# Optimization experiments

Measured on AMD Instinct MI355X. Metric: run time of the kernel, lower is better.

## Reference

```python
import jax, jax.numpy as jnp
import numpy as np

DEPTH, DIM, HEADS, MLP_HID, POS_DIM, PROJ_DIM, NCLS, INP = 5, 128, 8, 256, 128, 128, 1000, 35
EPS = 1e-5

def _ln(x, g, b):
    m = x.mean(-1, keepdims=True)
    v = ((x - m) ** 2).mean(-1, keepdims=True)
    return (x - m) / jnp.sqrt(v + EPS) * g + b

def _gelu(x):
    return jax.nn.gelu(x, approximate=False)  # torch nn.GELU default (erf)

def setup_inputs() -> dict:
    key = jax.random.key(0)
    ks = iter(jax.random.split(key, 80))
    nxt = lambda: next(ks)
    B, N = 8, 1024
    w = lambda *s: (jax.random.normal(nxt(), s, jnp.float32) / np.sqrt(s[-2]).astype(np.float32))
    z = lambda *s: jnp.zeros(s, jnp.float32)
    o = lambda *s: jnp.ones(s, jnp.float32)
    node_feat = jax.random.normal(nxt(), (B, N, 3), jnp.float32)
    a = (jax.random.uniform(nxt(), (B, N, N)) < 0.01).astype(jnp.float32)
    adj = jnp.maximum(a, a.transpose(0, 2, 1))  # symmetric 0/1 adjacency
    lapl = jax.random.normal(nxt(), (B, N, 32), jnp.float32) * 0.1
    d = dict(
        node_feat=node_feat, adj=adj, lapl=lapl,
        cls_token=jax.random.normal(nxt(), (1, 1, DIM), jnp.float32),
        pe_w1=w(INP, 2 * INP), pe_b1=z(2 * INP),
        pe_w2=w(2 * INP, 2 * INP), pe_b2=z(2 * INP),
        pe_w3=w(2 * INP, 2 * INP), pe_b3=z(2 * INP),
        pe_lng=o(2 * INP), pe_lnb=z(2 * INP),
        pe_w4=w(2 * INP, POS_DIM), pe_b4=z(POS_DIM),
        blk_ln1_g=o(DEPTH, DIM), blk_ln1_b=z(DEPTH, DIM),
        blk_qkv_w=w(DEPTH, DIM, 3 * HEADS * DIM),
        blk_proj_w=w(DEPTH, HEADS * DIM, DIM), blk_proj_b=z(DEPTH, DIM),
        blk_gamma_w=jax.random.uniform(nxt(), (DEPTH, DIM, 2), jnp.float32) * 0.01,
        blk_gamma_b=z(DEPTH, 2),
        blk_ln2_g=o(DEPTH, DIM), blk_ln2_b=z(DEPTH, DIM),
        blk_mlp_w1=w(DEPTH, DIM, MLP_HID), blk_mlp_b1=z(DEPTH, MLP_HID),
        blk_mlp_w2=w(DEPTH, MLP_HID, DIM), blk_mlp_b2=z(DEPTH, DIM),
        head_lng=o(DIM), head_lnb=z(DIM), head_w=w(DIM, DIM), head_b=z(DIM),
        proj_w1=w(DIM, PROJ_DIM), proj_b1=z(PROJ_DIM),
        proj_w2=w(PROJ_DIM, PROJ_DIM), proj_b2=z(PROJ_DIM),
        proj_w3=w(PROJ_DIM, PROJ_DIM), proj_b3=z(PROJ_DIM),
        proj_lng=o(PROJ_DIM), proj_lnb=z(PROJ_DIM),
        proj_w4=w(PROJ_DIM, NCLS), proj_b4=z(NCLS),
    )
    return d

def reference(node_feat, adj, lapl, cls_token, pe_w1, pe_b1, pe_w2, pe_b2, pe_w3, pe_b3,
              pe_lng, pe_lnb, pe_w4, pe_b4, blk_ln1_g, blk_ln1_b, blk_qkv_w, blk_proj_w,
              blk_proj_b, blk_gamma_w, blk_gamma_b, blk_ln2_g, blk_ln2_b, blk_mlp_w1,
              blk_mlp_b1, blk_mlp_w2, blk_mlp_b2, head_lng, head_lnb, head_w, head_b,
              proj_w1, proj_b1, proj_w2, proj_b2, proj_w3, proj_b3, proj_lng, proj_lnb,
              proj_w4, proj_b4):
    B, N, _ = node_feat.shape
    M = N + 1
    # positional-encoding MLP on concatenated [node_feat | lapl] (inp_dim = 35)
    x = jnp.concatenate([node_feat, lapl], axis=2)
    x = _gelu(x @ pe_w1 + pe_b1)
    x = _gelu(x @ pe_w2 + pe_b2)
    x = _gelu(x @ pe_w3 + pe_b3)
    x = _ln(x, pe_lng, pe_lnb) @ pe_w4 + pe_b4  # [B,N,DIM]
    x = jnp.concatenate([jnp.broadcast_to(cls_token, (B, 1, DIM)), x], axis=1)  # [B,M,DIM]
    # adjacency with cls row/col, adj_cls[:,0,0] = 1
    adj_cls = jnp.zeros((B, M, M), x.dtype).at[:, 0, 0].set(1.0).at[:, 1:, 1:].set(adj)
    scale = DIM ** (-0.5)
    for i in range(DEPTH):
        h = _ln(x, blk_ln1_g[i], blk_ln1_b[i])
        qkv = (h @ blk_qkv_w[i]).reshape(B, M, 3, HEADS, DIM).transpose(2, 0, 3, 1, 4)
        q, k, v = qkv[0], qkv[1], qkv[2]  # each [B,H,M,D]
        attn = jnp.einsum('bhnd,bhmd->bhnm', q, k) * scale
        gamma = jnp.exp(h @ blk_gamma_w[i] + blk_gamma_b[i])  # [B,M,2], use_exp=True
        attn = gamma[:, None, :, 0:1] * attn + gamma[:, None, :, 1:2] * adj_cls[:, None]
        attn = jax.nn.softmax(attn, axis=-1)
        o = jnp.einsum('bhnm,bhmd->bhnd', attn, v).transpose(0, 2, 1, 3).reshape(B, M, HEADS * DIM)
        x = o @ blk_proj_w[i] + blk_proj_b[i] + h  # residual from normed input (as in source)
        h2 = _ln(x, blk_ln2_g[i], blk_ln2_b[i])
        x = _gelu(h2 @ blk_mlp_w1[i] + blk_mlp_b1[i]) @ blk_mlp_w2[i] + blk_mlp_b2[i] + h2
    c = x[:, 0]
    c = _ln(c, head_lng, head_lnb) @ head_w + head_b  # mlp_head
    p = _gelu(c @ proj_w1 + proj_b1)
    p = _gelu(p @ proj_w2 + proj_b2)
    p = _gelu(p @ proj_w3 + proj_b3)
    p = _ln(p, proj_lng, proj_lnb) @ proj_w4 + proj_b4
    return (c, p)
```

## Files before the change

kernel.cpp:

```cpp
#include <hip/hip_runtime.h>
#include <hip/hip_bf16.h>
#include <math.h>

#define NB 8
#define NSEQ 1024
#define M_ 1025
#define ROWS (NB * M_)
#define DIMC 128
#define NHEADS 8
#define QKV3 3072
#define PEROWS (NB * NSEQ)
#define ACS 1088

typedef __attribute__((ext_vector_type(8))) short bf16x8;
typedef __attribute__((ext_vector_type(4))) float f32x4;

__device__ __forceinline__ float gelu_f(float x) {
  return 0.5f * x * (1.f + erff(x * 0.70710678118654752440f));
}

__device__ __forceinline__ unsigned short f2bf(float f) {
  __hip_bfloat16 h = __float2bfloat16(f);
  return *reinterpret_cast<unsigned short*>(&h);
}

__device__ __forceinline__ float bf2f(unsigned short u) {
  union { unsigned int i; float f; } c;
  c.i = ((unsigned int)u) << 16;
  return c.f;
}

template<int TR>
__global__ __launch_bounds__(256) void rowgemm_k(
    const float* __restrict__ in, const float* __restrict__ W,
    const float* __restrict__ bias, const float* __restrict__ res,
    float* __restrict__ out, int rows, int K, int Nout, int act, int remap)
{
  extern __shared__ float s_in[];
  const int tid = threadIdx.x;
  const int r0 = blockIdx.x * TR;
  const int tot = TR * K;
  for (int idx = tid; idx < tot; idx += blockDim.x) {
    int r = idx / K;
    int k = idx - r * K;
    int gr = r0 + r;
    s_in[idx] = (gr < rows) ? in[(size_t)gr * K + k] : 0.f;
  }
  __syncthreads();
  const int j = blockIdx.y * blockDim.x + tid;
  if (j >= Nout) return;
  float acc[TR];
  const float bv = bias ? bias[j] : 0.f;
#pragma unroll
  for (int r = 0; r < TR; ++r) acc[r] = bv;
  for (int k = 0; k < K; ++k) {
    const float w = W[(size_t)k * Nout + j];
#pragma unroll
    for (int r = 0; r < TR; ++r) acc[r] = fmaf(s_in[r * K + k], w, acc[r]);
  }
  for (int r = 0; r < TR; ++r) {
    const int gr = r0 + r;
    if (gr >= rows) break;
    float v = acc[r];
    if (act == 1) v = gelu_f(v);
    if (res) v += res[(size_t)gr * Nout + j];
    const size_t orow = remap ? (size_t)(gr + gr / 1024 + 1) : (size_t)gr;
    out[orow * (size_t)Nout + j] = v;
  }
}

template<int ACT, int OBF, int RES>
__global__ __launch_bounds__(256) void mgemm_k(
    const unsigned short* __restrict__ Xb, const unsigned short* __restrict__ Wt,
    const float* __restrict__ bias, const float* __restrict__ res,
    void* __restrict__ outp, int rows, int K, int N)
{
  __shared__ unsigned short sX[64][72];
  __shared__ unsigned short sW[64][72];
  const int tid = threadIdx.x;
  const int w = tid >> 6, lane = tid & 63;
  const int col = lane & 15, quad = lane >> 4;
  const int r0 = blockIdx.x * 64, n0 = blockIdx.y * 64;
  const int lr = tid >> 2, lc = tid & 3;
  const int xrow = min(r0 + lr, rows - 1);
  const unsigned short* xsrc = Xb + (size_t)xrow * K + lc * 8;
  const unsigned short* wsrc = Wt + (size_t)(n0 + lr) * K + lc * 8;

  f32x4 acc[4];
#pragma unroll
  for (int t = 0; t < 4; ++t) acc[t] = (f32x4){0.f, 0.f, 0.f, 0.f};

  for (int k0 = 0; k0 < K; k0 += 64) {
    __syncthreads();
    *(uint4*)&sX[lr][lc * 8]      = *(const uint4*)(xsrc + k0);
    *(uint4*)&sX[lr][lc * 8 + 32] = *(const uint4*)(xsrc + k0 + 32);
    *(uint4*)&sW[lr][lc * 8]      = *(const uint4*)(wsrc + k0);
    *(uint4*)&sW[lr][lc * 8 + 32] = *(const uint4*)(wsrc + k0 + 32);
    __syncthreads();
    const bf16x8 aX0 = *(const bf16x8*)&sX[w * 16 + col][quad * 8];
    const bf16x8 aX1 = *(const bf16x8*)&sX[w * 16 + col][32 + quad * 8];
#pragma unroll
    for (int t = 0; t < 4; ++t) {
      const bf16x8 bW0 = *(const bf16x8*)&sW[t * 16 + col][quad * 8];
      const bf16x8 bW1 = *(const bf16x8*)&sW[t * 16 + col][32 + quad * 8];
      acc[t] = __builtin_amdgcn_mfma_f32_16x16x32_bf16(aX0, bW0, acc[t], 0, 0, 0);
      acc[t] = __builtin_amdgcn_mfma_f32_16x16x32_bf16(aX1, bW1, acc[t], 0, 0, 0);
    }
  }
  const int gr_base = r0 + w * 16 + quad * 4;
#pragma unroll
  for (int t = 0; t < 4; ++t) {
    const int n = n0 + t * 16 + col;
    const float bv = bias ? bias[n] : 0.f;
#pragma unroll
    for (int r = 0; r < 4; ++r) {
      const int gr = gr_base + r;
      if (gr < rows) {
        float v = acc[t][r] + bv;
        if (ACT) v = gelu_f(v);
        if (RES) v += res[(size_t)gr * N + n];
        if (OBF) ((unsigned short*)outp)[(size_t)gr * N + n] = f2bf(v);
        else     ((float*)outp)[(size_t)gr * N + n] = v;
      }
    }
  }
}

__global__ __launch_bounds__(256) void ln_rows_k(
    const float* __restrict__ in, float* __restrict__ out,
    unsigned short* __restrict__ outb,
    const float* __restrict__ g, const float* __restrict__ b,
    const float* __restrict__ gw, const float* __restrict__ gb,
    float* __restrict__ gamout, int rows, int D)
{
  const int wv = (blockIdx.x * blockDim.x + threadIdx.x) >> 6;
  const int lane = threadIdx.x & 63;
  if (wv >= rows) return;
  const float* r = in + (size_t)wv * D;
  float s = 0.f;
  for (int d = lane; d < D; d += 64) s += r[d];
  for (int off = 32; off; off >>= 1) s += __shfl_down(s, off);
  const float mean = __shfl(s, 0) / (float)D;
  float v = 0.f;
  for (int d = lane; d < D; d += 64) { float t = r[d] - mean; v += t * t; }
  for (int off = 32; off; off >>= 1) v += __shfl_down(v, off);
  const float inv = rsqrtf(__shfl(v, 0) / (float)D + 1e-5f);
  float* orow = out + (size_t)wv * D;
  float a0 = 0.f, a1 = 0.f;
  for (int d = lane; d < D; d += 64) {
    const float o = (r[d] - mean) * inv * g[d] + b[d];
    orow[d] = o;
    if (outb) outb[(size_t)wv * D + d] = f2bf(o);
    if (gw) { a0 = fmaf(o, gw[2 * d], a0); a1 = fmaf(o, gw[2 * d + 1], a1); }
  }
  if (gw) {
    for (int off = 32; off; off >>= 1) { a0 += __shfl_down(a0, off); a1 += __shfl_down(a1, off); }
    if (lane == 0) {
      gamout[(size_t)wv * 2 + 0] = expf(a0 + gb[0]);
      gamout[(size_t)wv * 2 + 1] = expf(a1 + gb[1]);
    }
  }
}

__global__ void adjc_k(const float* __restrict__ adj, unsigned short* __restrict__ adjc)
{
  const int n = blockIdx.x;
  const int b = blockIdx.y;
  unsigned short* row = adjc + ((size_t)b * M_ + n) * ACS;
  const float* ar = (n >= 1) ? adj + ((size_t)b * NSEQ + (n - 1)) * NSEQ : nullptr;
  for (int m = threadIdx.x; m < ACS; m += 256) {
    float v = 0.f;
    if (n == 0) v = (m == 0) ? 1.f : 0.f;
    else if (m >= 1 && m <= NSEQ) v = ar[m - 1];
    row[m] = f2bf(v);
  }
}

__global__ void wtrans_k(const float* __restrict__ W, unsigned short* __restrict__ Wt,
                         int K, int N)
{
  __shared__ float t[32][33];
  const int k0 = blockIdx.x * 32, n0 = blockIdx.y * 32;
  const float* Wd = W + (size_t)blockIdx.z * K * N;
  unsigned short* Wtd = Wt + (size_t)blockIdx.z * K * N;
  for (int i = threadIdx.y; i < 32; i += 8)
    t[i][threadIdx.x] = Wd[(size_t)(k0 + i) * N + n0 + threadIdx.x];
  __syncthreads();
  for (int i = threadIdx.y; i < 32; i += 8)
    Wtd[(size_t)(n0 + i) * K + k0 + threadIdx.x] = f2bf(t[threadIdx.x][i]);
}

__global__ __launch_bounds__(256) void attn_mfma_k(
    const unsigned short* __restrict__ qkv, const float* __restrict__ gamma,
    const unsigned short* __restrict__ adjc, unsigned short* __restrict__ o)
{
  __shared__ unsigned short sK[64][136];
  __shared__ unsigned short sVt[128][72];
  __shared__ unsigned short sP[64][72];

  const int hh = blockIdx.x, qt = blockIdx.y, b = blockIdx.z;
  const int tid = threadIdx.x;
  const int w = tid >> 6;
  const int lane = tid & 63;
  const int col = lane & 15;
  const int quad = lane >> 4;
  const int n0 = qt * 64;
  const int qbase = n0 + w * 16;
  const float scale = 0.088388347648318447f;

  bf16x8 aQ[4];
  {
    const int qrow = min(qbase + col, 1024);
    const unsigned short* qp = qkv + ((size_t)(b * M_ + qrow)) * QKV3 + hh * DIMC + quad * 8;
#pragma unroll
    for (int c = 0; c < 4; ++c) aQ[c] = *(const bf16x8*)(qp + c * 32);
  }
  float g0[4], g1[4];
  const unsigned short* adjr[4];
#pragma unroll
  for (int r = 0; r < 4; ++r) {
    const int nc = min(qbase + quad * 4 + r, 1024);
    g0[r] = gamma[(size_t)(b * M_ + nc) * 2 + 0] * scale;
    g1[r] = gamma[(size_t)(b * M_ + nc) * 2 + 1];
    adjr[r] = adjc + ((size_t)b * M_ + nc) * ACS;
  }

  float l_i[4] = {0.f, 0.f, 0.f, 0.f};
  f32x4 Oacc[8];
#pragma unroll
  for (int t = 0; t < 8; ++t) Oacc[t] = (f32x4){0.f, 0.f, 0.f, 0.f};

  for (int kt = 0; kt < 17; ++kt) {
    const int m0 = kt * 64;
    __syncthreads();
#pragma unroll
    for (int l = 0; l < 4; ++l) {
      const int idx = l * 256 + tid;
      const int m = idx >> 4, c = idx & 15;
      const int gm = m0 + m;
      uint4 kv = make_uint4(0u, 0u, 0u, 0u), vv = make_uint4(0u, 0u, 0u, 0u);
      if (gm < M_) {
        const unsigned short* base = qkv + ((size_t)(b * M_ + gm)) * QKV3 + hh * DIMC + c * 8;
        kv = *(const uint4*)(base + 1024);
        vv = *(const uint4*)(base + 2048);
      }
      *(uint4*)&sK[m][c * 8] = kv;
      union { uint4 u; unsigned short s[8]; } vu; vu.u = vv;
      const int swcol = (((m >> 3) ^ (c & 7)) << 3) | (m & 7);
#pragma unroll
      for (int j = 0; j < 8; ++j) sVt[c * 8 + j][swcol] = vu.s[j];
    }
    __syncthreads();

    f32x4 Sacc[4];
#pragma unroll
    for (int t = 0; t < 4; ++t) Sacc[t] = (f32x4){0.f, 0.f, 0.f, 0.f};
#pragma unroll
    for (int t = 0; t < 4; ++t) {
#pragma unroll
      for (int c = 0; c < 4; ++c) {
        const bf16x8 bK = *(const bf16x8*)&sK[t * 16 + col][c * 32 + quad * 8];
        Sacc[t] = __builtin_amdgcn_mfma_f32_16x16x32_bf16(aQ[c], bK, Sacc[t], 0, 0, 0);
      }
    }

#pragma unroll
    for (int t = 0; t < 4; ++t) {
      const int m = m0 + t * 16 + col;
      const bool mv = (m < M_);
      const int chb = t * 2 + (col >> 3);
#pragma unroll
      for (int r = 0; r < 4; ++r) {
        const float av = bf2f(adjr[r][m]);
        const float s = fmaf(g0[r], Sacc[t][r], g1[r] * av);
        const float pv = mv ? __expf(s) : 0.f;
        l_i[r] += pv;
        const int ql = w * 16 + quad * 4 + r;
        sP[ql][((chb ^ (ql & 7)) * 8) + (col & 7)] = f2bf(pv);
      }
    }

#pragma unroll
    for (int ch = 0; ch < 2; ++ch) {
      const int r0a = w * 16 + col;
      const bf16x8 aP = *(const bf16x8*)&sP[r0a][(((ch * 4 + quad) ^ (col & 7)) * 8)];
#pragma unroll
      for (int t = 0; t < 8; ++t) {
        const int pc = (ch * 4 + quad) ^ ((t * 2 + (col >> 3)) & 7);
        const bf16x8 bV = *(const bf16x8*)&sVt[t * 16 + col][pc * 8];
        Oacc[t] = __builtin_amdgcn_mfma_f32_16x16x32_bf16(aP, bV, Oacc[t], 0, 0, 0);
      }
    }
  }

#pragma unroll
  for (int r = 0; r < 4; ++r) {
    float s = l_i[r];
    s += __shfl_xor(s, 1);
    s += __shfl_xor(s, 2);
    s += __shfl_xor(s, 4);
    s += __shfl_xor(s, 8);
    const int n = qbase + quad * 4 + r;
    if (n < M_) {
      const float invl = 1.f / s;
      unsigned short* orow = o + ((size_t)(b * M_ + n)) * (NHEADS * DIMC) + hh * DIMC + col;
#pragma unroll
      for (int t = 0; t < 8; ++t) orow[t * 16] = f2bf(Oacc[t][r] * invl);
    }
  }
}

__global__ void concat_pe_k(const float* __restrict__ nf, const float* __restrict__ lp,
                            float* __restrict__ x35, int rows)
{
  const int idx = blockIdx.x * blockDim.x + threadIdx.x;
  if (idx >= rows * 35) return;
  const int r = idx / 35, c = idx - r * 35;
  x35[idx] = (c < 3) ? nf[(size_t)r * 3 + c] : lp[(size_t)r * 32 + (c - 3)];
}

__global__ void fill_cls_k(const float* __restrict__ cls, float* __restrict__ x)
{
  x[(size_t)blockIdx.x * M_ * DIMC + threadIdx.x] = cls[threadIdx.x];
}

__global__ void extract_cls_k(const float* __restrict__ x, float* __restrict__ c0)
{
  c0[(size_t)blockIdx.x * DIMC + threadIdx.x] = x[(size_t)blockIdx.x * M_ * DIMC + threadIdx.x];
}

extern "C" void kernel_launch(void* const* d_in, const int* in_sizes, int n_in,
                              void* d_out, int out_size, void* d_ws, size_t ws_size,
                              hipStream_t stream)
{
  (void)in_sizes; (void)n_in; (void)out_size; (void)ws_size;
  const float* node_feat = (const float*)d_in[0];
  const float* adj       = (const float*)d_in[1];
  const float* lapl      = (const float*)d_in[2];
  const float* cls_token = (const float*)d_in[3];
  const float* pe_w1 = (const float*)d_in[4];
  const float* pe_b1 = (const float*)d_in[5];
  const float* pe_w2 = (const float*)d_in[6];
  const float* pe_b2 = (const float*)d_in[7];
  const float* pe_w3 = (const float*)d_in[8];
  const float* pe_b3 = (const float*)d_in[9];
  const float* pe_lng = (const float*)d_in[10];
  const float* pe_lnb = (const float*)d_in[11];
  const float* pe_w4 = (const float*)d_in[12];
  const float* pe_b4 = (const float*)d_in[13];
  const float* blk_ln1_g = (const float*)d_in[14];
  const float* blk_ln1_b = (const float*)d_in[15];
  const float* blk_qkv_w = (const float*)d_in[16];
  const float* blk_proj_w = (const float*)d_in[17];
  const float* blk_proj_b = (const float*)d_in[18];
  const float* blk_gamma_w = (const float*)d_in[19];
  const float* blk_gamma_b = (const float*)d_in[20];
  const float* blk_ln2_g = (const float*)d_in[21];
  const float* blk_ln2_b = (const float*)d_in[22];
  const float* blk_mlp_w1 = (const float*)d_in[23];
  const float* blk_mlp_b1 = (const float*)d_in[24];
  const float* blk_mlp_w2 = (const float*)d_in[25];
  const float* blk_mlp_b2 = (const float*)d_in[26];
  const float* head_lng = (const float*)d_in[27];
  const float* head_lnb = (const float*)d_in[28];
  const float* head_w = (const float*)d_in[29];
  const float* head_b = (const float*)d_in[30];
  const float* proj_w1 = (const float*)d_in[31];
  const float* proj_b1 = (const float*)d_in[32];
  const float* proj_w2 = (const float*)d_in[33];
  const float* proj_b2 = (const float*)d_in[34];
  const float* proj_w3 = (const float*)d_in[35];
  const float* proj_b3 = (const float*)d_in[36];
  const float* proj_lng = (const float*)d_in[37];
  const float* proj_lnb = (const float*)d_in[38];
  const float* proj_w4 = (const float*)d_in[39];
  const float* proj_b4 = (const float*)d_in[40];

  float* ws   = (float*)d_ws;
  float* x    = ws;
  float* h    = x + 1049600;
  float* gam  = h + 1049600;
  float* obuf = gam + 16400;
  unsigned short* obufb = (unsigned short*)obuf;
  unsigned short* hidb  = (unsigned short*)(obuf + 4198400);
  float* x35 = obuf;
  float* xa  = obuf + 300000;
  float* xb  = obuf + 900000;
  float* sm  = obuf + 5248000;
  unsigned short* hb   = (unsigned short*)(sm + 8192);
  unsigned short* qkv  = hb + 1049600;
  unsigned short* adjc = qkv + 25190400;
  unsigned short* qkvWt = adjc + 8921600;
  unsigned short* projWt = qkvWt + 5 * 393216;
  unsigned short* mlp1Wt = projWt + 5 * 131072;
  unsigned short* mlp2Wt = mlp1Wt + 5 * 32768;
  float* s0 = sm, *s1 = sm + 1024, *s2 = sm + 2048, *s3 = sm + 3072;

  float* out_c = (float*)d_out;
  float* out_p = out_c + NB * DIMC;

  adjc_k<<<dim3(M_, NB), 256, 0, stream>>>(adj, adjc);
  wtrans_k<<<dim3(4, 96, 5), dim3(32, 8), 0, stream>>>(blk_qkv_w, qkvWt, 128, 3072);
  wtrans_k<<<dim3(32, 4, 5), dim3(32, 8), 0, stream>>>(blk_proj_w, projWt, 1024, 128);
  wtrans_k<<<dim3(4, 8, 5), dim3(32, 8), 0, stream>>>(blk_mlp_w1, mlp1Wt, 128, 256);
  wtrans_k<<<dim3(8, 4, 5), dim3(32, 8), 0, stream>>>(blk_mlp_w2, mlp2Wt, 256, 128);

  concat_pe_k<<<(PEROWS * 35 + 255) / 256, 256, 0, stream>>>(node_feat, lapl, x35, PEROWS);
  rowgemm_k<16><<<dim3(512, 1), 128, 16 * 35 * 4, stream>>>(x35, pe_w1, pe_b1, nullptr, xa, PEROWS, 35, 70, 1, 0);
  rowgemm_k<16><<<dim3(512, 1), 128, 16 * 70 * 4, stream>>>(xa, pe_w2, pe_b2, nullptr, xb, PEROWS, 70, 70, 1, 0);
  rowgemm_k<16><<<dim3(512, 1), 128, 16 * 70 * 4, stream>>>(xb, pe_w3, pe_b3, nullptr, xa, PEROWS, 70, 70, 1, 0);
  ln_rows_k<<<(PEROWS * 64 + 255) / 256, 256, 0, stream>>>(xa, xb, nullptr, pe_lng, pe_lnb, nullptr, nullptr, nullptr, PEROWS, 70);
  rowgemm_k<16><<<dim3(512, 1), 128, 16 * 70 * 4, stream>>>(xb, pe_w4, pe_b4, nullptr, x, PEROWS, 70, DIMC, 0, 1);
  fill_cls_k<<<NB, DIMC, 0, stream>>>(cls_token, x);

  const int lnGrid = (ROWS * 64 + 255) / 256;
  for (int i = 0; i < 5; ++i) {
    const float* ln1g = blk_ln1_g + i * DIMC;
    const float* ln1b = blk_ln1_b + i * DIMC;
    const float* pb   = blk_proj_b + i * DIMC;
    const float* gw   = blk_gamma_w + (size_t)i * DIMC * 2;
    const float* gb   = blk_gamma_b + i * 2;
    const float* ln2g = blk_ln2_g + i * DIMC;
    const float* ln2b = blk_ln2_b + i * DIMC;
    const float* mb1  = blk_mlp_b1 + i * 256;
    const float* mb2  = blk_mlp_b2 + i * DIMC;
    const unsigned short* qw = qkvWt + (size_t)i * 393216;
    const unsigned short* pw = projWt + (size_t)i * 131072;
    const unsigned short* m1w = mlp1Wt + (size_t)i * 32768;
    const unsigned short* m2w = mlp2Wt + (size_t)i * 32768;

    ln_rows_k<<<lnGrid, 256, 0, stream>>>(x, h, hb, ln1g, ln1b, gw, gb, gam, ROWS, DIMC);
    mgemm_k<0, 1, 0><<<dim3(129, 48), 256, 0, stream>>>(hb, qw, nullptr, nullptr, qkv, ROWS, 128, 3072);
    attn_mfma_k<<<dim3(NHEADS, 17, NB), 256, 0, stream>>>(qkv, gam, adjc, obufb);
    mgemm_k<0, 0, 1><<<dim3(129, 2), 256, 0, stream>>>(obufb, pw, pb, h, x, ROWS, 1024, 128);
    ln_rows_k<<<lnGrid, 256, 0, stream>>>(x, h, hb, ln2g, ln2b, nullptr, nullptr, nullptr, ROWS, DIMC);
    mgemm_k<1, 1, 0><<<dim3(129, 4), 256, 0, stream>>>(hb, m1w, mb1, nullptr, hidb, ROWS, 128, 256);
    mgemm_k<0, 0, 1><<<dim3(129, 2), 256, 0, stream>>>(hidb, m2w, mb2, h, x, ROWS, 256, 128);
  }

  extract_cls_k<<<NB, DIMC, 0, stream>>>(x, s0);
  ln_rows_k<<<2, 256, 0, stream>>>(s0, s1, nullptr, head_lng, head_lnb, nullptr, nullptr, nullptr, NB, DIMC);
  rowgemm_k<8><<<dim3(1, 1), 128, 8 * 128 * 4, stream>>>(s1, head_w, head_b, nullptr, out_c, NB, DIMC, DIMC, 0, 0);
  rowgemm_k<8><<<dim3(1, 1), 128, 8 * 128 * 4, stream>>>(out_c, proj_w1, proj_b1, nullptr, s2, NB, DIMC, DIMC, 1, 0);
  rowgemm_k<8><<<dim3(1, 1), 128, 8 * 128 * 4, stream>>>(s2, proj_w2, proj_b2, nullptr, s3, NB, DIMC, DIMC, 1, 0);
  rowgemm_k<8><<<dim3(1, 1), 128, 8 * 128 * 4, stream>>>(s3, proj_w3, proj_b3, nullptr, s2, NB, DIMC, DIMC, 1, 0);
  ln_rows_k<<<2, 256, 0, stream>>>(s2, s3, nullptr, proj_lng, proj_lnb, nullptr, nullptr, nullptr, NB, DIMC);
  rowgemm_k<8><<<dim3(1, 4), 256, 8 * 128 * 4, stream>>>(s3, proj_w4, proj_b4, nullptr, out_p, NB, DIMC, 1000, 0, 0);
}
```

Baseline: 1.601 ms.

## Pre-transpose V into global layout and read K/V directly from global in attention

Adds a separate kernel that transposes the V slice of qkv into a per-(batch,head) [D][M] bf16 buffer. The attention kernel then drops its shared-memory K and V staging and both __syncthreads per tile, loading K fragments and transposed V fragments straight from global memory into MFMA operands. This removes the LDS scatter transpose and barriers, but adds an extra kernel launch and extra global traffic. It also relies on L2/cache to serve the K/V rows that all four waves now load redundantly. The padded tail of the V transpose (columns up to 1088) is zero-filled so masked keys stay harmless.

```diff
diff --git a/kernel.cpp b/kernel.cpp
--- a/kernel.cpp
+++ b/kernel.cpp
@@ -190,12 +190,39 @@
     Wtd[(size_t)(n0 + i) * K + k0 + threadIdx.x] = f2bf(t[threadIdx.x][i]);
 }
 
+__global__ __launch_bounds__(256) void vtrans_k(
+    const unsigned short* __restrict__ qkv, unsigned short* __restrict__ vt)
+{
+  __shared__ unsigned short sT[64][136];
+  const int mt = blockIdx.x, hh = blockIdx.y, b = blockIdx.z;
+  const int tid = threadIdx.x;
+  const int m0 = mt * 64;
+#pragma unroll
+  for (int l = 0; l < 4; ++l) {
+    const int idx = l * 256 + tid;
+    const int m = idx >> 4, c = idx & 15;
+    const int gm = m0 + m;
+    uint4 v = make_uint4(0u, 0u, 0u, 0u);
+    if (gm < M_) v = *(const uint4*)(qkv + ((size_t)(b * M_ + gm)) * QKV3 + 2048 + hh * DIMC + c * 8);
+    *(uint4*)&sT[m][c * 8] = v;
+  }
+  __syncthreads();
+#pragma unroll
+  for (int l = 0; l < 4; ++l) {
+    const int idx = l * 256 + tid;
+    const int d = idx >> 3, mc = idx & 7;
+    unsigned short tmp[8];
+#pragma unroll
+    for (int j = 0; j < 8; ++j) tmp[j] = sT[mc * 8 + j][d];
+    *(uint4*)(vt + (((size_t)(b * NHEADS + hh) * DIMC + d) * ACS) + m0 + mc * 8) = *(uint4*)tmp;
+  }
+}
+
 __global__ __launch_bounds__(256) void attn_mfma_k(
     const unsigned short* __restrict__ qkv, const float* __restrict__ gamma,
-    const unsigned short* __restrict__ adjc, unsigned short* __restrict__ o)
-{
-  __shared__ unsigned short sK[64][136];
-  __shared__ unsigned short sVt[128][72];
+    const unsigned short* __restrict__ adjc, const unsigned short* __restrict__ vt,
+    unsigned short* __restrict__ o)
+{
   __shared__ unsigned short sP[64][72];
 
   const int hh = blockIdx.x, qt = blockIdx.y, b = blockIdx.z;
@@ -230,36 +257,23 @@
 #pragma unroll
   for (int t = 0; t < 8; ++t) Oacc[t] = (f32x4){0.f, 0.f, 0.f, 0.f};
 
+  const size_t kcoloff = 1024 + hh * DIMC + quad * 8;
+  const unsigned short* vtb = vt + ((size_t)(b * NHEADS + hh)) * DIMC * ACS
+                              + (size_t)col * ACS + quad * 8;
+
   for (int kt = 0; kt < 17; ++kt) {
     const int m0 = kt * 64;
-    __syncthreads();
-#pragma unroll
-    for (int l = 0; l < 4; ++l) {
-      const int idx = l * 256 + tid;
-      const int m = idx >> 4, c = idx & 15;
-      const int gm = m0 + m;
-      uint4 kv = make_uint4(0u, 0u, 0u, 0u), vv = make_uint4(0u, 0u, 0u, 0u);
-      if (gm < M_) {
-        const unsigned short* base = qkv + ((size_t)(b * M_ + gm)) * QKV3 + hh * DIMC + c * 8;
-        kv = *(const uint4*)(base + 1024);
-        vv = *(const uint4*)(base + 2048);
-      }
-      *(uint4*)&sK[m][c * 8] = kv;
-      union { uint4 u; unsigned short s[8]; } vu; vu.u = vv;
-      const int swcol = (((m >> 3) ^ (c & 7)) << 3) | (m & 7);
-#pragma unroll
-      for (int j = 0; j < 8; ++j) sVt[c * 8 + j][swcol] = vu.s[j];
-    }
-    __syncthreads();
 
     f32x4 Sacc[4];
 #pragma unroll
     for (int t = 0; t < 4; ++t) Sacc[t] = (f32x4){0.f, 0.f, 0.f, 0.f};
 #pragma unroll
     for (int t = 0; t < 4; ++t) {
+      const int krow = min(m0 + t * 16 + col, 1024);
+      const unsigned short* kp = qkv + (size_t)(b * M_ + krow) * QKV3 + kcoloff;
 #pragma unroll
       for (int c = 0; c < 4; ++c) {
-        const bf16x8 bK = *(const bf16x8*)&sK[t * 16 + col][c * 32 + quad * 8];
+        const bf16x8 bK = *(const bf16x8*)(kp + c * 32);
         Sacc[t] = __builtin_amdgcn_mfma_f32_16x16x32_bf16(aQ[c], bK, Sacc[t], 0, 0, 0);
       }
     }
@@ -286,8 +300,7 @@
       const bf16x8 aP = *(const bf16x8*)&sP[r0a][(((ch * 4 + quad) ^ (col & 7)) * 8)];
 #pragma unroll
       for (int t = 0; t < 8; ++t) {
-        const int pc = (ch * 4 + quad) ^ ((t * 2 + (col >> 3)) & 7);
-        const bf16x8 bV = *(const bf16x8*)&sVt[t * 16 + col][pc * 8];
+        const bf16x8 bV = *(const bf16x8*)(vtb + (size_t)(t * 16) * ACS + m0 + ch * 32);
         Oacc[t] = __builtin_amdgcn_mfma_f32_16x16x32_bf16(aP, bV, Oacc[t], 0, 0, 0);
       }
     }
@@ -390,7 +403,8 @@
   unsigned short* hb   = (unsigned short*)(sm + 8192);
   unsigned short* qkv  = hb + 1049600;
   unsigned short* adjc = qkv + 25190400;
-  unsigned short* qkvWt = adjc + 8921600;
+  unsigned short* vt   = adjc + 8921600;
+  unsigned short* qkvWt = vt + 8912896;
   unsigned short* projWt = qkvWt + 5 * 393216;
   unsigned short* mlp1Wt = projWt + 5 * 131072;
   unsigned short* mlp2Wt = mlp1Wt + 5 * 32768;
@@ -431,7 +445,8 @@
 
     ln_rows_k<<<lnGrid, 256, 0, stream>>>(x, h, hb, ln1g, ln1b, gw, gb, gam, ROWS, DIMC);
     mgemm_k<0, 1, 0><<<dim3(129, 48), 256, 0, stream>>>(hb, qw, nullptr, nullptr, qkv, ROWS, 128, 3072);
-    attn_mfma_k<<<dim3(NHEADS, 17, NB), 256, 0, stream>>>(qkv, gam, adjc, obufb);
+    vtrans_k<<<dim3(17, NHEADS, NB), 256, 0, stream>>>(qkv, vt);
+    attn_mfma_k<<<dim3(NHEADS, 17, NB), 256, 0, stream>>>(qkv, gam, adjc, vt, obufb);
     mgemm_k<0, 0, 1><<<dim3(129, 2), 256, 0, stream>>>(obufb, pw, pb, h, x, ROWS, 1024, 128);
     ln_rows_k<<<lnGrid, 256, 0, stream>>>(x, h, hb, ln2g, ln2b, nullptr, nullptr, nullptr, ROWS, DIMC);
     mgemm_k<1, 1, 0><<<dim3(129, 4), 256, 0, stream>>>(hb, m1w, mb1, nullptr, hidb, ROWS, 128, 256);
```

After: 3.092 ms. +93.1%, slower.
